# Performance work log

Measured on AMD Instinct MI355X. Metric: run time of the kernel, lower is better.

## Reference

```python
import jax, jax.numpy as jnp
import numpy as np

N, B, T, D = 4, 4, 512, 512
H, DK, DV = 8, 64, 64
LN_EPS = 1e-5


def setup_inputs() -> dict:
    key = jax.random.key(0)
    ks = jax.random.split(key, 5)
    s = 1.0 / np.sqrt(D)
    return {
        "x": jax.random.normal(ks[0], (N, B, T, D), jnp.float32),
        "Wq": jax.random.normal(ks[1], (D, H * DK), jnp.float32) * s,
        "bq": jnp.zeros((H * DK,), jnp.float32),
        "Wk": jax.random.normal(ks[2], (D, H * DK), jnp.float32) * s,
        "bk": jnp.zeros((H * DK,), jnp.float32),
        "Wv": jax.random.normal(ks[3], (D, H * DV), jnp.float32) * s,
        "bv": jnp.zeros((H * DV,), jnp.float32),
        "Wo": jax.random.normal(ks[4], (H * DV, D), jnp.float32) * (1.0 / np.sqrt(H * DV)),
        "bo": jnp.zeros((D,), jnp.float32),
        "gamma": jnp.ones((D,), jnp.float32),
        "beta": jnp.zeros((D,), jnp.float32),
    }


def reference(x, Wq, bq, Wk, bk, Wv, bv, Wo, bo, gamma, beta):
    # x: [N, B, T, D] -- N variables, each [B, T, D]
    n = x.shape[0]
    # Project once per variable (the torch code redundantly recomputes K/V per query var).
    q = (x @ Wq + bq).reshape(n, B, T, H, DK).transpose(0, 1, 3, 2, 4)  # [N,B,H,T,DK]
    k = (x @ Wk + bk).reshape(n, B, T, H, DK).transpose(0, 1, 3, 2, 4)  # [N,B,H,T,DK]
    v = (x @ Wv + bv).reshape(n, B, T, H, DV).transpose(0, 1, 3, 2, 4)  # [N,B,H,T,DV]
    # All-pairs attention: softmax over keys of EACH key-variable separately.
    scores = jnp.einsum('qbhtk,cbhsk->qcbhts', q, k) / np.sqrt(DK)  # [Nq,Nc,B,H,T,T]
    attn = jax.nn.softmax(scores, axis=-1)
    ctx = jnp.einsum('qcbhts,cbhsv->qcbhtv', attn, v)  # [Nq,Nc,B,H,T,DV]
    ctx = ctx.transpose(0, 1, 2, 4, 3, 5).reshape(n, n, B, T, H * DV)
    out = ctx @ Wo + bo                     # per-pair output projection
    out = out.sum(axis=1) / n               # average over key variables -> [N,B,T,D]
    res = x + out
    mu = res.mean(axis=-1, keepdims=True)
    var = res.var(axis=-1, keepdims=True)
    y = (res - mu) / jnp.sqrt(var + LN_EPS) * gamma + beta
    return y
```

## Files before the change

kernel.cpp:

```cpp
#include <hip/hip_runtime.h>


typedef __bf16 bf16x8 __attribute__((ext_vector_type(8)));
typedef __bf16 bf16x4 __attribute__((ext_vector_type(4)));
typedef short shortx4 __attribute__((ext_vector_type(4)));
typedef float floatx4 __attribute__((ext_vector_type(4)));
typedef float floatx16 __attribute__((ext_vector_type(16)));
typedef unsigned short ushortx8 __attribute__((ext_vector_type(8)));

static __device__ __forceinline__ unsigned short f2bf(float f) {
  union { __bf16 h; unsigned short u; } c; c.h = (__bf16)f; return c.u;
}
static __device__ __forceinline__ float bf2f(unsigned short u) {
  union { unsigned u32; float f; } c; c.u32 = ((unsigned)u) << 16; return c.f;
}

#define QSCALE 0.18033688011112042f
#define SHIFT2 (-17.312340489609306f)

__global__ __launch_bounds__(256) void transpose_w(
    const float* __restrict__ W0, const float* __restrict__ W1,
    const float* __restrict__ W2, const float* __restrict__ W3,
    unsigned short* __restrict__ T0, unsigned short* __restrict__ T1,
    unsigned short* __restrict__ T2, unsigned short* __restrict__ T3)
{
  __shared__ unsigned short lds[64][65];
  const float* W; unsigned short* T;
  if (blockIdx.z == 0)      { W = W0; T = T0; }
  else if (blockIdx.z == 1) { W = W1; T = T1; }
  else if (blockIdx.z == 2) { W = W2; T = T2; }
  else                      { W = W3; T = T3; }
  const int xx = threadIdx.x;
  const int yy = threadIdx.y;
  const int k0 = blockIdx.x * 64, n0 = blockIdx.y * 64;
#pragma unroll
  for (int i = 0; i < 16; ++i) {
    const int row = yy * 16 + i;
    lds[row][xx] = f2bf(W[(size_t)(k0 + row) * 512 + n0 + xx]);
  }
  __syncthreads();
#pragma unroll
  for (int i = 0; i < 16; ++i) {
    const int nr = yy * 16 + i;
    T[(size_t)(n0 + nr) * 512 + k0 + xx] = lds[xx][nr];
  }
}

__global__ __launch_bounds__(256) void gemm_qkv(
    const float* __restrict__ X,
    const unsigned short* __restrict__ BT,
    const float* __restrict__ bq, const float* __restrict__ bk,
    const float* __restrict__ bv,
    unsigned short* __restrict__ Qo, unsigned short* __restrict__ Ko,
    unsigned short* __restrict__ Vo)
{
  __shared__ __align__(16) unsigned short lA[64][72];
  __shared__ __align__(16) unsigned short lB[64][72];
  const int tid  = threadIdx.x;
  const int wv   = tid >> 6, lane = tid & 63;
  const int quad = lane >> 4, l16 = lane & 15;
  const int m0 = blockIdx.x * 64, n0g = blockIdx.y * 64;
  const int sel = n0g >> 9;
  const int n0  = n0g & 511;
  const float* bias = (sel == 0) ? bq : (sel == 1) ? bk : bv;
  unsigned short* outp = (sel == 0) ? Qo : (sel == 1) ? Ko : Vo;
  const float scale = (sel == 0) ? QSCALE : 1.0f;
  floatx4 acc[4] = {};
  const int lrow = tid >> 2, lc0 = (tid & 3) * 16;

  for (int kc = 0; kc < 512; kc += 64) {
    __syncthreads();
    const float* as = X + (size_t)(m0 + lrow) * 512 + kc + lc0;
    float4 a0 = *(const float4*)as,       a1 = *(const float4*)(as + 4);
    float4 a2 = *(const float4*)(as + 8), a3 = *(const float4*)(as + 12);
    ushortx8 p0, p1;
    p0[0]=f2bf(a0.x); p0[1]=f2bf(a0.y); p0[2]=f2bf(a0.z); p0[3]=f2bf(a0.w);
    p0[4]=f2bf(a1.x); p0[5]=f2bf(a1.y); p0[6]=f2bf(a1.z); p0[7]=f2bf(a1.w);
    p1[0]=f2bf(a2.x); p1[1]=f2bf(a2.y); p1[2]=f2bf(a2.z); p1[3]=f2bf(a2.w);
    p1[4]=f2bf(a3.x); p1[5]=f2bf(a3.y); p1[6]=f2bf(a3.z); p1[7]=f2bf(a3.w);
    *(ushortx8*)&lA[lrow][lc0]     = p0;
    *(ushortx8*)&lA[lrow][lc0 + 8] = p1;
    const unsigned short* bs = BT + (size_t)(n0g + lrow) * 512 + kc + lc0;
    *(bf16x8*)&lB[lrow][lc0]     = *(const bf16x8*)bs;
    *(bf16x8*)&lB[lrow][lc0 + 8] = *(const bf16x8*)(bs + 8);
    __syncthreads();
    bf16x8 a0f = *(const bf16x8*)&lA[wv * 16 + l16][quad * 8];
    bf16x8 a1f = *(const bf16x8*)&lA[wv * 16 + l16][32 + quad * 8];
#pragma unroll
    for (int ni = 0; ni < 4; ++ni) {
      bf16x8 b0 = *(const bf16x8*)&lB[ni * 16 + l16][quad * 8];
      bf16x8 b1 = *(const bf16x8*)&lB[ni * 16 + l16][32 + quad * 8];
      acc[ni] = __builtin_amdgcn_mfma_f32_16x16x32_bf16(a0f, b0, acc[ni], 0, 0, 0);
      acc[ni] = __builtin_amdgcn_mfma_f32_16x16x32_bf16(a1f, b1, acc[ni], 0, 0, 0);
    }
  }

  const int mbase = m0 + wv * 16 + quad * 4;
#pragma unroll
  for (int ni = 0; ni < 4; ++ni) {
    const int nl = n0 + ni * 16 + l16;
    const float bvv = bias[nl];
    const int hh = nl >> 6, dk = nl & 63;
#pragma unroll
    for (int r = 0; r < 4; ++r) {
      const int m = mbase + r;
      const int nb = m >> 9, t = m & 511;
      const float v = (acc[ni][r] + bvv) * scale;
      if (sel == 2)
        outp[((size_t)(nb * 8 + hh) * 64 + dk) * 512 + t] = f2bf(v);
      else
        outp[((size_t)(nb * 8 + hh) * 512 + t) * 64 + dk] = f2bf(v);
    }
  }
}

__global__ __launch_bounds__(256) void gemm_out(
    const unsigned short* __restrict__ A,
    const unsigned short* __restrict__ BT,
    float* __restrict__ Cout)
{
  __shared__ __align__(16) unsigned short lA[64][72];
  __shared__ __align__(16) unsigned short lB[64][72];
  const int tid  = threadIdx.x;
  const int wv   = tid >> 6, lane = tid & 63;
  const int quad = lane >> 4, l16 = lane & 15;
  const int m0 = blockIdx.x * 64, n0 = blockIdx.y * 64;
  floatx4 acc[4] = {};
  const int lrow = tid >> 2, lc0 = (tid & 3) * 16;

  for (int kc = 0; kc < 512; kc += 64) {
    __syncthreads();
    const unsigned short* as = A + (size_t)(m0 + lrow) * 512 + kc + lc0;
    *(bf16x8*)&lA[lrow][lc0]     = *(const bf16x8*)as;
    *(bf16x8*)&lA[lrow][lc0 + 8] = *(const bf16x8*)(as + 8);
    const unsigned short* bs = BT + (size_t)(n0 + lrow) * 512 + kc + lc0;
    *(bf16x8*)&lB[lrow][lc0]     = *(const bf16x8*)bs;
    *(bf16x8*)&lB[lrow][lc0 + 8] = *(const bf16x8*)(bs + 8);
    __syncthreads();
    bf16x8 a0 = *(const bf16x8*)&lA[wv * 16 + l16][quad * 8];
    bf16x8 a1 = *(const bf16x8*)&lA[wv * 16 + l16][32 + quad * 8];
#pragma unroll
    for (int ni = 0; ni < 4; ++ni) {
      bf16x8 b0 = *(const bf16x8*)&lB[ni * 16 + l16][quad * 8];
      bf16x8 b1 = *(const bf16x8*)&lB[ni * 16 + l16][32 + quad * 8];
      acc[ni] = __builtin_amdgcn_mfma_f32_16x16x32_bf16(a0, b0, acc[ni], 0, 0, 0);
      acc[ni] = __builtin_amdgcn_mfma_f32_16x16x32_bf16(a1, b1, acc[ni], 0, 0, 0);
    }
  }
  const int mbase = m0 + wv * 16 + quad * 4;
#pragma unroll
  for (int ni = 0; ni < 4; ++ni) {
    const int n = n0 + ni * 16 + l16;
#pragma unroll
    for (int r = 0; r < 4; ++r)
      Cout[(size_t)(mbase + r) * 512 + n] = acc[ni][r];
  }
}

__global__ __launch_bounds__(256) void flash_kernel(
    const unsigned short* __restrict__ Q,
    const unsigned short* __restrict__ K,
    const unsigned short* __restrict__ VT,
    unsigned short* __restrict__ CTX2)
{
  __shared__ __align__(16) unsigned short lK[2][64][72];
  __shared__ __align__(16) unsigned short lV[2][64][68];
  const int tid  = threadIdx.x;
  const int wv   = tid >> 6, lane = tid & 63;
  const int l32  = lane & 31, u = lane >> 5;

  const int lin  = blockIdx.x;
  const int xcd  = lin & 7, slot = lin >> 3;
  const int tile = slot & 3;
  const int nbh  = xcd * 16 + ((slot >> 2) & 15);
  const int cg   = slot >> 6;
  const int t0   = tile * 128;
  const int h = nbh & 7, nb = nbh >> 3, b = nb & 3;

  const unsigned short* qbase = Q + ((size_t)nbh * 512 + (t0 + wv * 32 + l32)) * 64;
  bf16x8 qf[4];
#pragma unroll
  for (int c16 = 0; c16 < 4; ++c16)
    qf[c16] = *(const bf16x8*)(qbase + c16 * 16 + u * 8);

  const int srow = tid >> 2, sc0 = (tid & 3) * 16;
  const unsigned short *kptr, *vptr;
  auto setptr = [&](int it) {
    const int c = cg * 2 + (it >> 3), s0 = (it & 7) * 64;
    const size_t kvbh = (size_t)((c * 4 + b) * 8 + h);
    kptr = K  + kvbh * (512 * 64) + (size_t)(s0 + srow) * 64 + sc0;
    vptr = VT + kvbh * (64 * 512) + (size_t)srow * 512 + s0 + sc0;
  };
  bf16x8 rk0, rk1, rv0, rv1;
  auto loadregs = [&]() {
    rk0 = *(const bf16x8*)kptr; rk1 = *(const bf16x8*)(kptr + 8);
    rv0 = *(const bf16x8*)vptr; rv1 = *(const bf16x8*)(vptr + 8);
  };
  auto writebuf = [&](int p) {
    *(bf16x8*)&lK[p][srow][sc0]     = rk0;
    *(bf16x8*)&lK[p][srow][sc0 + 8] = rk1;
    union { bf16x8 v8; bf16x4 v4[2]; } c0, c1;
    c0.v8 = rv0; c1.v8 = rv1;
    *(bf16x4*)&lV[p][srow][sc0]      = c0.v4[0];
    *(bf16x4*)&lV[p][srow][sc0 + 4]  = c0.v4[1];
    *(bf16x4*)&lV[p][srow][sc0 + 8]  = c1.v4[0];
    *(bf16x4*)&lV[p][srow][sc0 + 12] = c1.v4[1];
  };

  setptr(0); loadregs();
  writebuf(0);
  setptr(1); loadregs();
  __syncthreads();

  floatx16 ofin0 = {}, ofin1 = {};
  floatx16 oc0, oc1;
  float lacc;

  for (int it = 0; it < 16; ++it) {
    const int cur = it & 1;
    const int st = it & 7;
    if (st == 0) { oc0 = floatx16{}; oc1 = floatx16{}; lacc = 0.f; }

    if (it < 15) writebuf(cur ^ 1);
    if (it < 14) { setptr(it + 2); loadregs(); }

    floatx16 sacc0, sacc1;
#pragma unroll
    for (int r = 0; r < 16; ++r) { sacc0[r] = SHIFT2; sacc1[r] = SHIFT2; }
#pragma unroll
    for (int c16 = 0; c16 < 4; ++c16) {
      bf16x8 ak0 = *(const bf16x8*)&lK[cur][l32][c16 * 16 + u * 8];
      bf16x8 ak1 = *(const bf16x8*)&lK[cur][32 + l32][c16 * 16 + u * 8];
      sacc0 = __builtin_amdgcn_mfma_f32_32x32x16_bf16(ak0, qf[c16], sacc0, 0, 0, 0);
      sacc1 = __builtin_amdgcn_mfma_f32_32x32x16_bf16(ak1, qf[c16], sacc1, 0, 0, 0);
    }

#pragma unroll
    for (int sb = 0; sb < 2; ++sb) {
      const floatx16& sa = sb ? sacc1 : sacc0;
#pragma unroll
      for (int c8 = 0; c8 < 4; ++c8) {
        float e0 = __builtin_amdgcn_exp2f(sa[4 * c8 + 0]);
        float e1 = __builtin_amdgcn_exp2f(sa[4 * c8 + 1]);
        float e2 = __builtin_amdgcn_exp2f(sa[4 * c8 + 2]);
        float e3 = __builtin_amdgcn_exp2f(sa[4 * c8 + 3]);
        lacc += (e0 + e1) + (e2 + e3);
        shortx4 pf;
        pf[0] = (short)f2bf(e0); pf[1] = (short)f2bf(e1);
        pf[2] = (short)f2bf(e2); pf[3] = (short)f2bf(e3);
        const int sloc = sb * 32 + c8 * 8 + u * 4;
        shortx4 vf0 = *(const shortx4*)&lV[cur][l32][sloc];
        shortx4 vf1 = *(const shortx4*)&lV[cur][32 + l32][sloc];
        oc0 = __builtin_amdgcn_mfma_f32_32x32x8bf16_1k(pf, vf0, oc0, 0, 0, 0);
        oc1 = __builtin_amdgcn_mfma_f32_32x32x8bf16_1k(pf, vf1, oc1, 0, 0, 0);
      }
    }

    if (st == 7) {
      float s = lacc;
      s += __shfl_xor(s, 32);
      const float inv = 1.0f / s;
#pragma unroll
      for (int r = 0; r < 16; ++r) {
        const int trow = (r & 3) + 8 * (r >> 2) + 4 * u;
        const float invr = __shfl(inv, trow);
        ofin0[r] += oc0[r] * invr;
        ofin1[r] += oc1[r] * invr;
      }
    }
    __syncthreads();
  }

  unsigned short* outp = CTX2 + (size_t)cg * (8192 * 512);
  const int mbase = nb * 512 + t0 + wv * 32;
#pragma unroll
  for (int r = 0; r < 16; ++r) {
    const int trow = (r & 3) + 8 * (r >> 2) + 4 * u;
    const size_t rowoff = (size_t)(mbase + trow) * 512 + h * 64;
    outp[rowoff + l32]      = f2bf(ofin0[r]);
    outp[rowoff + 32 + l32] = f2bf(ofin1[r]);
  }
}

__global__ __launch_bounds__(256) void reduce2(
    const unsigned short* __restrict__ A, const unsigned short* __restrict__ B,
    unsigned short* __restrict__ O)
{
  const size_t i = ((size_t)blockIdx.x * 256 + threadIdx.x) * 8;
  ushortx8 a = *(const ushortx8*)(A + i);
  ushortx8 b = *(const ushortx8*)(B + i);
  ushortx8 o;
#pragma unroll
  for (int j = 0; j < 8; ++j) o[j] = f2bf(bf2f(a[j]) + bf2f(b[j]));
  *(ushortx8*)(O + i) = o;
}

__global__ __launch_bounds__(256) void ln_kernel(
    const float* __restrict__ x, const float* __restrict__ tmp,
    const float* __restrict__ bo, const float* __restrict__ gamma,
    const float* __restrict__ beta, float* __restrict__ out)
{
  const int row = blockIdx.x;
  const int t = threadIdx.x;
  const size_t base = (size_t)row * 512;
  const float r0 = x[base + t]       + 0.25f * tmp[base + t]       + bo[t];
  const float r1 = x[base + t + 256] + 0.25f * tmp[base + t + 256] + bo[t + 256];
  float s = r0 + r1, sq = r0 * r0 + r1 * r1;
#pragma unroll
  for (int off = 1; off < 64; off <<= 1) {
    s  += __shfl_xor(s, off);
    sq += __shfl_xor(sq, off);
  }
  __shared__ float ls[4], lq[4];
  const int wv = t >> 6, lane = t & 63;
  if (lane == 0) { ls[wv] = s; lq[wv] = sq; }
  __syncthreads();
  s  = ls[0] + ls[1] + ls[2] + ls[3];
  sq = lq[0] + lq[1] + lq[2] + lq[3];
  const float mu  = s * (1.0f / 512.0f);
  const float var = sq * (1.0f / 512.0f) - mu * mu;
  const float inv = rsqrtf(var + 1e-5f);
  out[base + t]       = (r0 - mu) * inv * gamma[t]       + beta[t];
  out[base + t + 256] = (r1 - mu) * inv * gamma[t + 256] + beta[t + 256];
}

extern "C" void kernel_launch(void* const* d_in, const int* in_sizes, int n_in,
                              void* d_out, int out_size, void* d_ws, size_t ws_size,
                              hipStream_t stream) {
  const float* x     = (const float*)d_in[0];
  const float* Wq    = (const float*)d_in[1];
  const float* bq    = (const float*)d_in[2];
  const float* Wk    = (const float*)d_in[3];
  const float* bk    = (const float*)d_in[4];
  const float* Wv    = (const float*)d_in[5];
  const float* bv    = (const float*)d_in[6];
  const float* Wo    = (const float*)d_in[7];
  const float* bo    = (const float*)d_in[8];
  const float* gamma = (const float*)d_in[9];
  const float* beta  = (const float*)d_in[10];
  float* out = (float*)d_out;

  char* w = (char*)d_ws;
  unsigned short* q_bf  = (unsigned short*)(w);
  unsigned short* k_bf  = (unsigned short*)(w + (size_t)8  * 1024 * 1024);
  unsigned short* vt_bf = (unsigned short*)(w + (size_t)16 * 1024 * 1024);
  unsigned short* ctx2  = (unsigned short*)(w + (size_t)24 * 1024 * 1024);
  unsigned short* wqkvT = (unsigned short*)(w + (size_t)40 * 1024 * 1024);
  unsigned short* woT   = wqkvT + 786432;
  unsigned short* ctx   = (unsigned short*)(w);
  float* tmp            = (float*)(w + (size_t)8 * 1024 * 1024);

  transpose_w<<<dim3(8, 8, 4), dim3(64, 4), 0, stream>>>(
      Wq, Wk, Wv, Wo, wqkvT, wqkvT + 262144, wqkvT + 524288, woT);
  gemm_qkv<<<dim3(128, 24), 256, 0, stream>>>(x, wqkvT, bq, bk, bv,
                                              q_bf, k_bf, vt_bf);
  flash_kernel<<<1024, 256, 0, stream>>>(q_bf, k_bf, vt_bf, ctx2);
  reduce2<<<2048, 256, 0, stream>>>(ctx2, ctx2 + (size_t)8192 * 512, ctx);
  gemm_out<<<dim3(128, 8), 256, 0, stream>>>(ctx, woT, tmp);
  ln_kernel<<<8192, 256, 0, stream>>>(x, tmp, bo, gamma, beta, out);
}
```

Measured before the change: 214.3 us.

## Enlarge GEMM tiles to 128x128, fuse reduce into out-proj, pre-convert x to bf16

The QKV and output-projection GEMMs move from 64x64 to 128x128 block tiles, with each wave computing a 64x64 sub-tile so that LDS fragments are reused more. The x-to-bf16 conversion moves into a prep kernel that also holds the weight transposes, replacing the separate transpose launch. The two-way bf16 context reduction is folded into the output GEMM's A-tile load, which removes the reduce2 kernel and one intermediate round-trip. Larger tiles cut the grid to 768 and 256 blocks and raise register use, so occupancy and SM fill can drop.

```diff
diff --git a/kernel.cpp b/kernel.cpp
--- a/kernel.cpp
+++ b/kernel.cpp
@@ -18,142 +18,180 @@
 #define QSCALE 0.18033688011112042f
 #define SHIFT2 (-17.312340489609306f)
 
-__global__ __launch_bounds__(256) void transpose_w(
-    const float* __restrict__ W0, const float* __restrict__ W1,
-    const float* __restrict__ W2, const float* __restrict__ W3,
-    unsigned short* __restrict__ T0, unsigned short* __restrict__ T1,
-    unsigned short* __restrict__ T2, unsigned short* __restrict__ T3)
-{
-  __shared__ unsigned short lds[64][65];
-  const float* W; unsigned short* T;
-  if (blockIdx.z == 0)      { W = W0; T = T0; }
-  else if (blockIdx.z == 1) { W = W1; T = T1; }
-  else if (blockIdx.z == 2) { W = W2; T = T2; }
-  else                      { W = W3; T = T3; }
-  const int xx = threadIdx.x;
-  const int yy = threadIdx.y;
-  const int k0 = blockIdx.x * 64, n0 = blockIdx.y * 64;
-#pragma unroll
-  for (int i = 0; i < 16; ++i) {
-    const int row = yy * 16 + i;
-    lds[row][xx] = f2bf(W[(size_t)(k0 + row) * 512 + n0 + xx]);
-  }
-  __syncthreads();
-#pragma unroll
-  for (int i = 0; i < 16; ++i) {
-    const int nr = yy * 16 + i;
-    T[(size_t)(n0 + nr) * 512 + k0 + xx] = lds[xx][nr];
+__global__ __launch_bounds__(256) void prep(
+    const float* __restrict__ Wq, const float* __restrict__ Wk,
+    const float* __restrict__ Wv, const float* __restrict__ Wo,
+    const float* __restrict__ x,
+    unsigned short* __restrict__ wqkvT, unsigned short* __restrict__ woT,
+    unsigned short* __restrict__ x_bf)
+{
+  const int bid = blockIdx.x;
+  const int tid = threadIdx.x;
+  if (bid < 256) {
+    __shared__ unsigned short lds[64][65];
+    const int z = bid >> 6, rest = bid & 63;
+    const int k0 = (rest >> 3) * 64, n0 = (rest & 7) * 64;
+    const float* W; unsigned short* T;
+    if (z == 0)      { W = Wq; T = wqkvT; }
+    else if (z == 1) { W = Wk; T = wqkvT + 262144; }
+    else if (z == 2) { W = Wv; T = wqkvT + 524288; }
+    else             { W = Wo; T = woT; }
+    const int xx = tid & 63, yy = tid >> 6;
+#pragma unroll
+    for (int i = 0; i < 16; ++i) {
+      const int row = yy * 16 + i;
+      lds[row][xx] = f2bf(W[(size_t)(k0 + row) * 512 + n0 + xx]);
+    }
+    __syncthreads();
+#pragma unroll
+    for (int i = 0; i < 16; ++i) {
+      const int nr = yy * 16 + i;
+      T[(size_t)(n0 + nr) * 512 + k0 + xx] = lds[xx][nr];
+    }
+  } else {
+    const int i = (bid - 256) * 256 + tid;
+    const float4 a = ((const float4*)x)[i * 2];
+    const float4 b = ((const float4*)x)[i * 2 + 1];
+    ushortx8 o;
+    o[0] = f2bf(a.x); o[1] = f2bf(a.y); o[2] = f2bf(a.z); o[3] = f2bf(a.w);
+    o[4] = f2bf(b.x); o[5] = f2bf(b.y); o[6] = f2bf(b.z); o[7] = f2bf(b.w);
+    *(ushortx8*)(x_bf + (size_t)i * 8) = o;
   }
 }
 
 __global__ __launch_bounds__(256) void gemm_qkv(
-    const float* __restrict__ X,
+    const unsigned short* __restrict__ Xb,
     const unsigned short* __restrict__ BT,
     const float* __restrict__ bq, const float* __restrict__ bk,
     const float* __restrict__ bv,
     unsigned short* __restrict__ Qo, unsigned short* __restrict__ Ko,
     unsigned short* __restrict__ Vo)
 {
-  __shared__ __align__(16) unsigned short lA[64][72];
-  __shared__ __align__(16) unsigned short lB[64][72];
+  __shared__ __align__(16) unsigned short lA[128][72];
+  __shared__ __align__(16) unsigned short lB[128][72];
   const int tid  = threadIdx.x;
   const int wv   = tid >> 6, lane = tid & 63;
   const int quad = lane >> 4, l16 = lane & 15;
-  const int m0 = blockIdx.x * 64, n0g = blockIdx.y * 64;
-  const int sel = n0g >> 9;
-  const int n0  = n0g & 511;
+  const int wm = wv >> 1, wn = wv & 1;
+  const int m0  = blockIdx.x * 128;
+  const int by  = blockIdx.y;
+  const int n0g = by * 128;
+  const int sel = by >> 2;
   const float* bias = (sel == 0) ? bq : (sel == 1) ? bk : bv;
+  const float scale = (sel == 0) ? QSCALE : 1.0f;
   unsigned short* outp = (sel == 0) ? Qo : (sel == 1) ? Ko : Vo;
-  const float scale = (sel == 0) ? QSCALE : 1.0f;
-  floatx4 acc[4] = {};
-  const int lrow = tid >> 2, lc0 = (tid & 3) * 16;
+
+  floatx4 acc[4][4] = {};
+  const int srow = tid >> 1, sc0 = (tid & 1) * 32;
 
   for (int kc = 0; kc < 512; kc += 64) {
     __syncthreads();
-    const float* as = X + (size_t)(m0 + lrow) * 512 + kc + lc0;
-    float4 a0 = *(const float4*)as,       a1 = *(const float4*)(as + 4);
-    float4 a2 = *(const float4*)(as + 8), a3 = *(const float4*)(as + 12);
-    ushortx8 p0, p1;
-    p0[0]=f2bf(a0.x); p0[1]=f2bf(a0.y); p0[2]=f2bf(a0.z); p0[3]=f2bf(a0.w);
-    p0[4]=f2bf(a1.x); p0[5]=f2bf(a1.y); p0[6]=f2bf(a1.z); p0[7]=f2bf(a1.w);
-    p1[0]=f2bf(a2.x); p1[1]=f2bf(a2.y); p1[2]=f2bf(a2.z); p1[3]=f2bf(a2.w);
-    p1[4]=f2bf(a3.x); p1[5]=f2bf(a3.y); p1[6]=f2bf(a3.z); p1[7]=f2bf(a3.w);
-    *(ushortx8*)&lA[lrow][lc0]     = p0;
-    *(ushortx8*)&lA[lrow][lc0 + 8] = p1;
-    const unsigned short* bs = BT + (size_t)(n0g + lrow) * 512 + kc + lc0;
-    *(bf16x8*)&lB[lrow][lc0]     = *(const bf16x8*)bs;
-    *(bf16x8*)&lB[lrow][lc0 + 8] = *(const bf16x8*)(bs + 8);
-    __syncthreads();
-    bf16x8 a0f = *(const bf16x8*)&lA[wv * 16 + l16][quad * 8];
-    bf16x8 a1f = *(const bf16x8*)&lA[wv * 16 + l16][32 + quad * 8];
+    const unsigned short* as = Xb + (size_t)(m0 + srow) * 512 + kc + sc0;
+    const unsigned short* bs = BT + (size_t)(n0g + srow) * 512 + kc + sc0;
+#pragma unroll
+    for (int j = 0; j < 4; ++j) {
+      *(bf16x8*)&lA[srow][sc0 + j * 8] = *(const bf16x8*)(as + j * 8);
+      *(bf16x8*)&lB[srow][sc0 + j * 8] = *(const bf16x8*)(bs + j * 8);
+    }
+    __syncthreads();
+    bf16x8 af[4][2];
+#pragma unroll
+    for (int ti = 0; ti < 4; ++ti) {
+      af[ti][0] = *(const bf16x8*)&lA[wm * 64 + ti * 16 + l16][quad * 8];
+      af[ti][1] = *(const bf16x8*)&lA[wm * 64 + ti * 16 + l16][32 + quad * 8];
+    }
 #pragma unroll
     for (int ni = 0; ni < 4; ++ni) {
-      bf16x8 b0 = *(const bf16x8*)&lB[ni * 16 + l16][quad * 8];
-      bf16x8 b1 = *(const bf16x8*)&lB[ni * 16 + l16][32 + quad * 8];
-      acc[ni] = __builtin_amdgcn_mfma_f32_16x16x32_bf16(a0f, b0, acc[ni], 0, 0, 0);
-      acc[ni] = __builtin_amdgcn_mfma_f32_16x16x32_bf16(a1f, b1, acc[ni], 0, 0, 0);
-    }
-  }
-
-  const int mbase = m0 + wv * 16 + quad * 4;
+      bf16x8 b0 = *(const bf16x8*)&lB[wn * 64 + ni * 16 + l16][quad * 8];
+      bf16x8 b1 = *(const bf16x8*)&lB[wn * 64 + ni * 16 + l16][32 + quad * 8];
+#pragma unroll
+      for (int ti = 0; ti < 4; ++ti) {
+        acc[ti][ni] = __builtin_amdgcn_mfma_f32_16x16x32_bf16(af[ti][0], b0, acc[ti][ni], 0, 0, 0);
+        acc[ti][ni] = __builtin_amdgcn_mfma_f32_16x16x32_bf16(af[ti][1], b1, acc[ti][ni], 0, 0, 0);
+      }
+    }
+  }
+
 #pragma unroll
   for (int ni = 0; ni < 4; ++ni) {
-    const int nl = n0 + ni * 16 + l16;
-    const float bvv = bias[nl];
-    const int hh = nl >> 6, dk = nl & 63;
-#pragma unroll
-    for (int r = 0; r < 4; ++r) {
-      const int m = mbase + r;
-      const int nb = m >> 9, t = m & 511;
-      const float v = (acc[ni][r] + bvv) * scale;
-      if (sel == 2)
-        outp[((size_t)(nb * 8 + hh) * 64 + dk) * 512 + t] = f2bf(v);
-      else
-        outp[((size_t)(nb * 8 + hh) * 512 + t) * 64 + dk] = f2bf(v);
+    const int n = (n0g & 511) + wn * 64 + ni * 16 + l16;
+    const float bvv = bias[n];
+    const int hh = n >> 6, dk = n & 63;
+#pragma unroll
+    for (int ti = 0; ti < 4; ++ti) {
+      const int mb = m0 + wm * 64 + ti * 16 + quad * 4;
+#pragma unroll
+      for (int r = 0; r < 4; ++r) {
+        const int m = mb + r;
+        const int nb = m >> 9, t = m & 511;
+        const float v = (acc[ti][ni][r] + bvv) * scale;
+        if (sel == 2)
+          outp[((size_t)(nb * 8 + hh) * 64 + dk) * 512 + t] = f2bf(v);
+        else
+          outp[((size_t)(nb * 8 + hh) * 512 + t) * 64 + dk] = f2bf(v);
+      }
     }
   }
 }
 
 __global__ __launch_bounds__(256) void gemm_out(
-    const unsigned short* __restrict__ A,
-    const unsigned short* __restrict__ BT,
-    float* __restrict__ Cout)
-{
-  __shared__ __align__(16) unsigned short lA[64][72];
-  __shared__ __align__(16) unsigned short lB[64][72];
+    const unsigned short* __restrict__ C0, const unsigned short* __restrict__ C1,
+    const unsigned short* __restrict__ BT, float* __restrict__ Cout)
+{
+  __shared__ __align__(16) unsigned short lA[128][72];
+  __shared__ __align__(16) unsigned short lB[128][72];
   const int tid  = threadIdx.x;
   const int wv   = tid >> 6, lane = tid & 63;
   const int quad = lane >> 4, l16 = lane & 15;
-  const int m0 = blockIdx.x * 64, n0 = blockIdx.y * 64;
-  floatx4 acc[4] = {};
-  const int lrow = tid >> 2, lc0 = (tid & 3) * 16;
+  const int wm = wv >> 1, wn = wv & 1;
+  const int m0 = blockIdx.x * 128, n0 = blockIdx.y * 128;
+
+  floatx4 acc[4][4] = {};
+  const int srow = tid >> 1, sc0 = (tid & 1) * 32;
 
   for (int kc = 0; kc < 512; kc += 64) {
     __syncthreads();
-    const unsigned short* as = A + (size_t)(m0 + lrow) * 512 + kc + lc0;
-    *(bf16x8*)&lA[lrow][lc0]     = *(const bf16x8*)as;
-    *(bf16x8*)&lA[lrow][lc0 + 8] = *(const bf16x8*)(as + 8);
-    const unsigned short* bs = BT + (size_t)(n0 + lrow) * 512 + kc + lc0;
-    *(bf16x8*)&lB[lrow][lc0]     = *(const bf16x8*)bs;
-    *(bf16x8*)&lB[lrow][lc0 + 8] = *(const bf16x8*)(bs + 8);
-    __syncthreads();
-    bf16x8 a0 = *(const bf16x8*)&lA[wv * 16 + l16][quad * 8];
-    bf16x8 a1 = *(const bf16x8*)&lA[wv * 16 + l16][32 + quad * 8];
+    const size_t aoff = (size_t)(m0 + srow) * 512 + kc + sc0;
+    const unsigned short* bs = BT + (size_t)(n0 + srow) * 512 + kc + sc0;
+#pragma unroll
+    for (int j = 0; j < 4; ++j) {
+      ushortx8 a0 = *(const ushortx8*)(C0 + aoff + j * 8);
+      ushortx8 a1 = *(const ushortx8*)(C1 + aoff + j * 8);
+      ushortx8 o;
+#pragma unroll
+      for (int e = 0; e < 8; ++e) o[e] = f2bf(bf2f(a0[e]) + bf2f(a1[e]));
+      *(ushortx8*)&lA[srow][sc0 + j * 8] = o;
+      *(bf16x8*)&lB[srow][sc0 + j * 8] = *(const bf16x8*)(bs + j * 8);
+    }
+    __syncthreads();
+    bf16x8 af[4][2];
+#pragma unroll
+    for (int ti = 0; ti < 4; ++ti) {
+      af[ti][0] = *(const bf16x8*)&lA[wm * 64 + ti * 16 + l16][quad * 8];
+      af[ti][1] = *(const bf16x8*)&lA[wm * 64 + ti * 16 + l16][32 + quad * 8];
+    }
 #pragma unroll
     for (int ni = 0; ni < 4; ++ni) {
-      bf16x8 b0 = *(const bf16x8*)&lB[ni * 16 + l16][quad * 8];
-      bf16x8 b1 = *(const bf16x8*)&lB[ni * 16 + l16][32 + quad * 8];
-      acc[ni] = __builtin_amdgcn_mfma_f32_16x16x32_bf16(a0, b0, acc[ni], 0, 0, 0);
-      acc[ni] = __builtin_amdgcn_mfma_f32_16x16x32_bf16(a1, b1, acc[ni], 0, 0, 0);
-    }
-  }
-  const int mbase = m0 + wv * 16 + quad * 4;
+      bf16x8 b0 = *(const bf16x8*)&lB[wn * 64 + ni * 16 + l16][quad * 8];
+      bf16x8 b1 = *(const bf16x8*)&lB[wn * 64 + ni * 16 + l16][32 + quad * 8];
+#pragma unroll
+      for (int ti = 0; ti < 4; ++ti) {
+        acc[ti][ni] = __builtin_amdgcn_mfma_f32_16x16x32_bf16(af[ti][0], b0, acc[ti][ni], 0, 0, 0);
+        acc[ti][ni] = __builtin_amdgcn_mfma_f32_16x16x32_bf16(af[ti][1], b1, acc[ti][ni], 0, 0, 0);
+      }
+    }
+  }
+
 #pragma unroll
   for (int ni = 0; ni < 4; ++ni) {
-    const int n = n0 + ni * 16 + l16;
-#pragma unroll
-    for (int r = 0; r < 4; ++r)
-      Cout[(size_t)(mbase + r) * 512 + n] = acc[ni][r];
+    const int n = n0 + wn * 64 + ni * 16 + l16;
+#pragma unroll
+    for (int ti = 0; ti < 4; ++ti) {
+      const int mb = m0 + wm * 64 + ti * 16 + quad * 4;
+#pragma unroll
+      for (int r = 0; r < 4; ++r)
+        Cout[(size_t)(mb + r) * 512 + n] = acc[ti][ni][r];
+    }
   }
 }
 
@@ -282,19 +320,6 @@
   }
 }
 
-__global__ __launch_bounds__(256) void reduce2(
-    const unsigned short* __restrict__ A, const unsigned short* __restrict__ B,
-    unsigned short* __restrict__ O)
-{
-  const size_t i = ((size_t)blockIdx.x * 256 + threadIdx.x) * 8;
-  ushortx8 a = *(const ushortx8*)(A + i);
-  ushortx8 b = *(const ushortx8*)(B + i);
-  ushortx8 o;
-#pragma unroll
-  for (int j = 0; j < 8; ++j) o[j] = f2bf(bf2f(a[j]) + bf2f(b[j]));
-  *(ushortx8*)(O + i) = o;
-}
-
 __global__ __launch_bounds__(256) void ln_kernel(
     const float* __restrict__ x, const float* __restrict__ tmp,
     const float* __restrict__ bo, const float* __restrict__ gamma,
@@ -344,18 +369,17 @@
   unsigned short* q_bf  = (unsigned short*)(w);
   unsigned short* k_bf  = (unsigned short*)(w + (size_t)8  * 1024 * 1024);
   unsigned short* vt_bf = (unsigned short*)(w + (size_t)16 * 1024 * 1024);
+  unsigned short* x_bf  = (unsigned short*)(w + (size_t)24 * 1024 * 1024);
   unsigned short* ctx2  = (unsigned short*)(w + (size_t)24 * 1024 * 1024);
   unsigned short* wqkvT = (unsigned short*)(w + (size_t)40 * 1024 * 1024);
   unsigned short* woT   = wqkvT + 786432;
-  unsigned short* ctx   = (unsigned short*)(w);
-  float* tmp            = (float*)(w + (size_t)8 * 1024 * 1024);
-
-  transpose_w<<<dim3(8, 8, 4), dim3(64, 4), 0, stream>>>(
-      Wq, Wk, Wv, Wo, wqkvT, wqkvT + 262144, wqkvT + 524288, woT);
-  gemm_qkv<<<dim3(128, 24), 256, 0, stream>>>(x, wqkvT, bq, bk, bv,
-                                              q_bf, k_bf, vt_bf);
+  float* tmp            = (float*)(w);
+
+  prep<<<2304, 256, 0, stream>>>(Wq, Wk, Wv, Wo, x, wqkvT, woT, x_bf);
+  gemm_qkv<<<dim3(64, 12), 256, 0, stream>>>(x_bf, wqkvT, bq, bk, bv,
+                                             q_bf, k_bf, vt_bf);
   flash_kernel<<<1024, 256, 0, stream>>>(q_bf, k_bf, vt_bf, ctx2);
-  reduce2<<<2048, 256, 0, stream>>>(ctx2, ctx2 + (size_t)8192 * 512, ctx);
-  gemm_out<<<dim3(128, 8), 256, 0, stream>>>(ctx, woT, tmp);
+  gemm_out<<<dim3(64, 4), 256, 0, stream>>>(ctx2, ctx2 + (size_t)8192 * 512,
+                                            woT, tmp);
   ln_kernel<<<8192, 256, 0, stream>>>(x, tmp, bo, gamma, beta, out);
 }
```

Result: faster. 197.6 us (-7.8%).
